# Optimization experiments

Measured on AMD Instinct MI355X. Metric: run time of the kernel, lower is better.

## Reference

```python
import jax, jax.numpy as jnp
import numpy as np

N_NODES, N_EDGES, N_GRAPHS = 50000, 500000, 64
NODE_D, EDGE_D, GLOB_D = 256, 128, 64
EPS = 1e-5


def setup_inputs() -> dict:
    key = jax.random.key(0)
    ks = jax.random.split(key, 12)
    inp = {
        "x": jax.random.normal(ks[0], (N_NODES, NODE_D), jnp.float32),
        "edge_attr": jax.random.normal(ks[1], (N_EDGES, EDGE_D), jnp.float32),
        "u": jax.random.normal(ks[2], (N_GRAPHS, GLOB_D), jnp.float32),
        "W1": jax.random.normal(ks[3], (NODE_D + EDGE_D, 4 * EDGE_D), jnp.float32) * 0.02,
        "b1": jnp.zeros((4 * EDGE_D,), jnp.float32),
        "W2": jax.random.normal(ks[4], (4 * EDGE_D, EDGE_D), jnp.float32) * 0.02,
        "b2": jnp.zeros((EDGE_D,), jnp.float32),
        "W3": jax.random.normal(ks[5], (NODE_D + EDGE_D + GLOB_D, 4 * NODE_D), jnp.float32) * 0.02,
        "b3": jnp.zeros((4 * NODE_D,), jnp.float32),
        "W4": jax.random.normal(ks[6], (4 * NODE_D, NODE_D), jnp.float32) * 0.02,
        "b4": jnp.zeros((NODE_D,), jnp.float32),
        "gamma": jnp.ones((NODE_D,), jnp.float32),
        "beta": jnp.zeros((NODE_D,), jnp.float32),
        "edge_index": jax.random.randint(ks[7], (2, N_EDGES), 0, N_NODES, jnp.int64 if jax.config.jax_enable_x64 else jnp.int32),
        "batch": jnp.sort(jax.random.randint(ks[8], (N_NODES,), 0, N_GRAPHS, jnp.int64 if jax.config.jax_enable_x64 else jnp.int32)),
    }
    return inp


def reference(x, edge_attr, u, W1, b1, W2, b2, W3, b3, W4, b4, gamma, beta, edge_index, batch):
    row, col = edge_index[0], edge_index[1]
    n = x.shape[0]
    # edge MLP on [x[row] || edge_attr]
    e = jnp.concatenate([x[row], edge_attr], axis=1)            # [E, node+edge]
    e = jnp.maximum(e @ W1 + b1, 0.0) @ W2 + b2                 # [E, edge]
    # scatter-mean by destination node
    s = jax.ops.segment_sum(e, col, num_segments=n)             # [N, edge]
    cnt = jax.ops.segment_sum(jnp.ones((col.shape[0],), x.dtype), col, num_segments=n)
    agg = s / jnp.maximum(cnt, 1.0)[:, None]
    # node update MLP on [x || agg || u[batch]]
    h = jnp.concatenate([x, agg, u[batch]], axis=1)             # [N, node+edge+glob]
    h = jnp.maximum(h @ W3 + b3, 0.0) @ W4 + b4                 # [N, node]
    # residual + layernorm (dropout p=0 -> identity)
    y = h + x
    mu = jnp.mean(y, axis=-1, keepdims=True)
    var = jnp.mean((y - mu) ** 2, axis=-1, keepdims=True)
    return (y - mu) * jax.lax.rsqrt(var + EPS) * gamma + beta
```

## Files before the change

### kernel.cpp

```cpp
#include <hip/hip_runtime.h>
#include <stdint.h>

#define NE 500000
#define NN 50000
#define ND 256
#define ED 128
#define GD 64
#define MAXDEG 64

typedef float f4v __attribute__((ext_vector_type(4)));
typedef short s8v __attribute__((ext_vector_type(8)));
typedef short s4v __attribute__((ext_vector_type(4)));

static __device__ __forceinline__ short f2bf(float f) {
  union { float f; uint32_t u; } v; v.f = f;
  uint32_t r = v.u + 0x7FFFu + ((v.u >> 16) & 1u);
  return (short)(r >> 16);
}
static __device__ __forceinline__ float bf2f(uint32_t u) {
  union { uint32_t u; float f; } v; v.u = u << 16; return v.f;
}

static __device__ __forceinline__ void pack_one(const float* __restrict__ src,
                                                short* __restrict__ dst, int C, int idx) {
  int k = idx / C, c = idx - k * C;
  int ks = k >> 5, kh = (k >> 3) & 3, j = k & 7;
  dst[(((ks * C + c) * 4 + kh) << 3) + j] = f2bf(src[idx]);
}

#define J0 3200000
#define J1 196608
#define J2 65536
#define J3 458752
#define J4 262144
#define J5 500000
__global__ void prep_kernel(const float* __restrict__ x, short* __restrict__ xbf,
                            const float* __restrict__ W1, const float* __restrict__ W2,
                            const float* __restrict__ W3, const float* __restrict__ W4,
                            short* __restrict__ w1p, short* __restrict__ w2p,
                            short* __restrict__ w3p, short* __restrict__ w4p,
                            const int* __restrict__ ecol, unsigned int* __restrict__ cnt,
                            int* __restrict__ elist) {
  int idx = blockIdx.x * blockDim.x + threadIdx.x;
  if (idx < J0) {
    int i = idx * 4;
    const float4 v = *(const float4*)(x + i);
    s4v o; o[0] = f2bf(v.x); o[1] = f2bf(v.y); o[2] = f2bf(v.z); o[3] = f2bf(v.w);
    *(s4v*)(xbf + i) = o;
    return;
  }
  idx -= J0;
  if (idx < J1) { pack_one(W1, w1p, 512, idx); return; }
  idx -= J1;
  if (idx < J2) { pack_one(W2, w2p, 128, idx); return; }
  idx -= J2;
  if (idx < J3) { pack_one(W3, w3p, 1024, idx); return; }
  idx -= J3;
  if (idx < J4) { pack_one(W4, w4p, 256, idx); return; }
  idx -= J4;
  if (idx < J5) {
    int c = ecol[idx];
    unsigned int slot = atomicAdd(&cnt[c], 1u);
    if (slot < MAXDEG) elist[c * MAXDEG + slot] = idx;
  }
}

__global__ void agg_kernel(const unsigned short* __restrict__ ebuf,
                           const int* __restrict__ elist,
                           const unsigned int* __restrict__ cnt,
                           unsigned short* __restrict__ aggbf) {
  int tid = threadIdx.x;
  int lane = tid & 63;
  int node = blockIdx.x * 4 + (tid >> 6);
  if (node >= NN) return;
  unsigned int deg = cnt[node];
  unsigned int jend = deg < MAXDEG ? deg : MAXDEG;
  float a0 = 0.f, a1 = 0.f;
  const int* el = elist + (size_t)node * MAXDEG;
  for (unsigned int j = 0; j < jend; ++j) {
    int eid = el[j];
    uint32_t v = *(const uint32_t*)(ebuf + (size_t)eid * ED + 2 * lane);
    a0 += bf2f(v & 0xFFFFu);
    a1 += bf2f(v >> 16);
  }
  float rc = 1.0f / (deg > 0 ? (float)deg : 1.0f);
  uint32_t o = (uint32_t)(uint16_t)f2bf(a0 * rc) | ((uint32_t)(uint16_t)f2bf(a1 * rc) << 16);
  *(uint32_t*)(aggbf + (size_t)node * ED + 2 * lane) = o;
}

__launch_bounds__(1024, 4)
__global__ void edge_kernel(const short* __restrict__ xbf,
                            const float* __restrict__ edge_attr,
                            const short* __restrict__ w1p,
                            const float* __restrict__ b1,
                            const short* __restrict__ w2p,
                            const float* __restrict__ b2,
                            const int* __restrict__ erow,
                            unsigned short* __restrict__ ebuf) {
  __shared__ __align__(16) short smem[128 * 384 + 128 * 256];
  char* const h1b = (char*)smem + 128 * 384 * 2;
  int* const rid = (int*)h1b;
  const int tid = threadIdx.x;
  const int lane = tid & 63;
  const int w = tid >> 6;
  const int lh = lane >> 4;
  const int ll = lane & 15;
  const int e0 = blockIdx.x * 128;

  if (tid < 128) {
    int e = e0 + tid;
    rid[tid] = (e < NE) ? erow[e] : 0;
  }
  __syncthreads();

  #pragma unroll
  for (int it = 0; it < 6; ++it) {
    int ch = tid + it * 1024;
    int rr = ch / 48;
    int cc = (ch - rr * 48) * 8;
    s8v vals = {0, 0, 0, 0, 0, 0, 0, 0};
    if (e0 + rr < NE) {
      if (cc < ND) {
        vals = *(const s8v*)(xbf + (size_t)rid[rr] * ND + cc);
      } else {
        const float* p = edge_attr + (size_t)(e0 + rr) * ED + (cc - ND);
        const float4 v0 = *(const float4*)(p);
        const float4 v1 = *(const float4*)(p + 4);
        vals[0] = f2bf(v0.x); vals[1] = f2bf(v0.y); vals[2] = f2bf(v0.z); vals[3] = f2bf(v0.w);
        vals[4] = f2bf(v1.x); vals[5] = f2bf(v1.y); vals[6] = f2bf(v1.z); vals[7] = f2bf(v1.w);
      }
    }
    int byte = (rr * 768 + cc * 2) ^ ((rr & 7) << 4);
    *(s8v*)((char*)smem + byte) = vals;
  }
  __syncthreads();

  f4v acc1[2][8];
  #pragma unroll
  for (int n = 0; n < 2; ++n)
    #pragma unroll
    for (int m = 0; m < 8; ++m)
      acc1[n][m] = (f4v){0.f, 0.f, 0.f, 0.f};

  for (int ks = 0; ks < 12; ++ks) {
    s8v wf0 = *(const s8v*)(w1p + (((ks * 512 + w * 16 + ll) * 4 + lh) << 3));
    s8v wf1 = *(const s8v*)(w1p + (((ks * 512 + 256 + w * 16 + ll) * 4 + lh) << 3));
    #pragma unroll
    for (int mh = 0; mh < 2; ++mh) {
      s8v hf[4];
      #pragma unroll
      for (int m = 0; m < 4; ++m) {
        int row = 64 * mh + 16 * m + ll;
        int byte = (row * 768 + ks * 64 + lh * 16) ^ ((row & 7) << 4);
        hf[m] = *(const s8v*)((const char*)smem + byte);
      }
      #pragma unroll
      for (int m = 0; m < 4; ++m) {
        acc1[0][4 * mh + m] = __builtin_amdgcn_mfma_f32_16x16x32_bf16(wf0, hf[m], acc1[0][4 * mh + m], 0, 0, 0);
        acc1[1][4 * mh + m] = __builtin_amdgcn_mfma_f32_16x16x32_bf16(wf1, hf[m], acc1[1][4 * mh + m], 0, 0, 0);
      }
    }
  }
  __syncthreads();

  f4v acc2[4];
  #pragma unroll
  for (int m = 0; m < 4; ++m)
    acc2[m] = (f4v){0.f, 0.f, 0.f, 0.f};

  #pragma unroll
  for (int half = 0; half < 2; ++half) {
    {
      int lcb = w * 16 + 4 * lh;
      const float4 bv = *(const float4*)(b1 + half * 256 + lcb);
      #pragma unroll
      for (int m = 0; m < 8; ++m) {
        int row = 16 * m + ll;
        s4v o;
        float v0 = acc1[half][m][0] + bv.x; o[0] = f2bf(v0 > 0.f ? v0 : 0.f);
        float v1 = acc1[half][m][1] + bv.y; o[1] = f2bf(v1 > 0.f ? v1 : 0.f);
        float v2 = acc1[half][m][2] + bv.z; o[2] = f2bf(v2 > 0.f ? v2 : 0.f);
        float v3 = acc1[half][m][3] + bv.w; o[3] = f2bf(v3 > 0.f ? v3 : 0.f);
        int byte = (row * 512 + lcb * 2) ^ ((row & 7) << 4);
        *(s4v*)(h1b + byte) = o;
      }
    }
    __syncthreads();

    for (int ksl = 0; ksl < 8; ++ksl) {
      int ksg = half * 8 + ksl;
      s8v wf = *(const s8v*)(w2p + (((ksg * 128 + (w & 7) * 16 + ll) * 4 + lh) << 3));
      #pragma unroll
      for (int m = 0; m < 4; ++m) {
        int row = 64 * (w >> 3) + 16 * m + ll;
        int byte = (row * 512 + ksl * 64 + lh * 16) ^ ((row & 7) << 4);
        s8v hf = *(const s8v*)(h1b + byte);
        acc2[m] = __builtin_amdgcn_mfma_f32_16x16x32_bf16(wf, hf, acc2[m], 0, 0, 0);
      }
    }
    __syncthreads();
  }

  {
    int cb = (w & 7) * 16 + 4 * lh;
    const float4 bv = *(const float4*)(b2 + cb);
    #pragma unroll
    for (int m = 0; m < 4; ++m) {
      int row = 64 * (w >> 3) + 16 * m + ll;
      s4v o;
      o[0] = f2bf(acc2[m][0] + bv.x);
      o[1] = f2bf(acc2[m][1] + bv.y);
      o[2] = f2bf(acc2[m][2] + bv.z);
      o[3] = f2bf(acc2[m][3] + bv.w);
      int byte = (row * 256 + cb * 2) ^ ((row & 7) << 4);
      *(s4v*)((char*)smem + byte) = o;
    }
  }
  __syncthreads();

  {
    size_t g0 = (size_t)e0 * ED;
    #pragma unroll
    for (int it = 0; it < 2; ++it) {
      int B = (tid + it * 1024) * 16;
      int row = B >> 8;
      int lb = B ^ ((row & 7) << 4);
      s8v v = *(const s8v*)((const char*)smem + lb);
      if (e0 + row < NE)
        *(s8v*)((char*)(ebuf + g0) + B) = v;
    }
  }
}

__launch_bounds__(1024, 4)
__global__ void node_kernel(const float* __restrict__ x,
                            const short* __restrict__ xbf,
                            const float* __restrict__ u,
                            const short* __restrict__ w3p,
                            const float* __restrict__ b3,
                            const short* __restrict__ w4p,
                            const float* __restrict__ b4,
                            const float* __restrict__ gamma,
                            const float* __restrict__ beta,
                            const int* __restrict__ batch,
                            const unsigned short* __restrict__ aggbf,
                            float* __restrict__ out) {
  __shared__ __align__(16) short smem[64 * 1024];
  const int tid = threadIdx.x;
  const int lane = tid & 63;
  const int w = tid >> 6;
  const int lh = lane >> 4;
  const int ll = lane & 15;
  const int n0 = blockIdx.x * 64;

  #pragma unroll
  for (int it = 0; it < 4; ++it) {
    int ch = tid + it * 1024;
    if (ch < 3584) {
      int rr = ch / 56;
      int cc = (ch - rr * 56) * 8;
      s8v vals = {0, 0, 0, 0, 0, 0, 0, 0};
      int node = n0 + rr;
      if (node < NN) {
        if (cc < 256) {
          vals = *(const s8v*)(xbf + (size_t)node * ND + cc);
        } else if (cc < 384) {
          vals = *(const s8v*)(aggbf + (size_t)node * ED + (cc - 256));
        } else {
          const float* up = u + (size_t)batch[node] * GD + (cc - 384);
          const float4 v0 = *(const float4*)(up);
          const float4 v1 = *(const float4*)(up + 4);
          vals[0] = f2bf(v0.x); vals[1] = f2bf(v0.y); vals[2] = f2bf(v0.z); vals[3] = f2bf(v0.w);
          vals[4] = f2bf(v1.x); vals[5] = f2bf(v1.y); vals[6] = f2bf(v1.z); vals[7] = f2bf(v1.w);
        }
      }
      int byte = (rr * 896 + cc * 2) ^ ((rr & 7) << 4);
      *(s8v*)((char*)smem + byte) = vals;
    }
  }
  __syncthreads();

  f4v acc3[4][4];
  #pragma unroll
  for (int n = 0; n < 4; ++n)
    #pragma unroll
    for (int m = 0; m < 4; ++m)
      acc3[n][m] = (f4v){0.f, 0.f, 0.f, 0.f};

  for (int ks = 0; ks < 14; ++ks) {
    s8v af[4];
    #pragma unroll
    for (int m = 0; m < 4; ++m) {
      int row = 16 * m + ll;
      int byte = (row * 896 + ks * 64 + lh * 16) ^ ((row & 7) << 4);
      af[m] = *(const s8v*)((const char*)smem + byte);
    }
    #pragma unroll
    for (int n = 0; n < 4; ++n) {
      s8v wf = *(const s8v*)(w3p + (((ks * 1024 + w * 64 + 16 * n + ll) * 4 + lh) << 3));
      #pragma unroll
      for (int m = 0; m < 4; ++m)
        acc3[n][m] = __builtin_amdgcn_mfma_f32_16x16x32_bf16(wf, af[m], acc3[n][m], 0, 0, 0);
    }
  }
  __syncthreads();

  #pragma unroll
  for (int n = 0; n < 4; ++n) {
    int cb = w * 64 + 16 * n + 4 * lh;
    const float4 bv = *(const float4*)(b3 + cb);
    #pragma unroll
    for (int m = 0; m < 4; ++m) {
      int row = 16 * m + ll;
      s4v o;
      float v0 = acc3[n][m][0] + bv.x; o[0] = f2bf(v0 > 0.f ? v0 : 0.f);
      float v1 = acc3[n][m][1] + bv.y; o[1] = f2bf(v1 > 0.f ? v1 : 0.f);
      float v2 = acc3[n][m][2] + bv.z; o[2] = f2bf(v2 > 0.f ? v2 : 0.f);
      float v3 = acc3[n][m][3] + bv.w; o[3] = f2bf(v3 > 0.f ? v3 : 0.f);
      int byte = (row * 2048 + cb * 2) ^ ((row & 7) << 4);
      *(s4v*)((char*)smem + byte) = o;
    }
  }
  __syncthreads();

  f4v acc4[4];
  #pragma unroll
  for (int m = 0; m < 4; ++m)
    acc4[m] = (f4v){0.f, 0.f, 0.f, 0.f};

  for (int ks = 0; ks < 32; ++ks) {
    s8v wf = *(const s8v*)(w4p + (((ks * 256 + w * 16 + ll) * 4 + lh) << 3));
    #pragma unroll
    for (int m = 0; m < 4; ++m) {
      int row = 16 * m + ll;
      int byte = (row * 2048 + ks * 64 + lh * 16) ^ ((row & 7) << 4);
      s8v hf = *(const s8v*)((const char*)smem + byte);
      acc4[m] = __builtin_amdgcn_mfma_f32_16x16x32_bf16(wf, hf, acc4[m], 0, 0, 0);
    }
  }
  __syncthreads();

  float* yb = (float*)smem;
  {
    int cb = w * 16 + 4 * lh;
    const float4 bv = *(const float4*)(b4 + cb);
    #pragma unroll
    for (int m = 0; m < 4; ++m) {
      int row = 16 * m + ll;
      int node = n0 + row;
      float4 xv = {0.f, 0.f, 0.f, 0.f};
      if (node < NN) xv = *(const float4*)(x + (size_t)node * ND + cb);
      f4v o;
      o[0] = acc4[m][0] + bv.x + xv.x;
      o[1] = acc4[m][1] + bv.y + xv.y;
      o[2] = acc4[m][2] + bv.z + xv.z;
      o[3] = acc4[m][3] + bv.w + xv.w;
      *(f4v*)(yb + row * 260 + cb) = o;
    }
  }
  __syncthreads();

  {
    int row = tid >> 4, sub = tid & 15;
    int node = n0 + row;
    float v[16];
    float sum = 0.f, ssq = 0.f;
    #pragma unroll
    for (int i = 0; i < 4; ++i) {
      const float4 t = *(const float4*)(yb + row * 260 + (i * 16 + sub) * 4);
      v[i * 4 + 0] = t.x; v[i * 4 + 1] = t.y; v[i * 4 + 2] = t.z; v[i * 4 + 3] = t.w;
      sum += t.x + t.y + t.z + t.w;
      ssq += t.x * t.x + t.y * t.y + t.z * t.z + t.w * t.w;
    }
    #pragma unroll
    for (int d = 1; d < 16; d <<= 1) {
      sum += __shfl_xor(sum, d);
      ssq += __shfl_xor(ssq, d);
    }
    float mu = sum * (1.f / 256.f);
    float var = ssq * (1.f / 256.f) - mu * mu;
    float rstd = rsqrtf(var + 1e-5f);
    if (node < NN) {
      #pragma unroll
      for (int i = 0; i < 4; ++i) {
        int c = (i * 16 + sub) * 4;
        const float4 g = *(const float4*)(gamma + c);
        const float4 be = *(const float4*)(beta + c);
        float4 o;
        o.x = (v[i * 4 + 0] - mu) * rstd * g.x + be.x;
        o.y = (v[i * 4 + 1] - mu) * rstd * g.y + be.y;
        o.z = (v[i * 4 + 2] - mu) * rstd * g.z + be.z;
        o.w = (v[i * 4 + 3] - mu) * rstd * g.w + be.w;
        *(float4*)(out + (size_t)node * ND + c) = o;
      }
    }
  }
}

extern "C" void kernel_launch(void* const* d_in, const int* in_sizes, int n_in,
                              void* d_out, int out_size, void* d_ws, size_t ws_size,
                              hipStream_t stream) {
  const float* x    = (const float*)d_in[0];
  const float* ea   = (const float*)d_in[1];
  const float* u    = (const float*)d_in[2];
  const float* W1   = (const float*)d_in[3];
  const float* b1   = (const float*)d_in[4];
  const float* W2   = (const float*)d_in[5];
  const float* b2   = (const float*)d_in[6];
  const float* W3   = (const float*)d_in[7];
  const float* b3   = (const float*)d_in[8];
  const float* W4   = (const float*)d_in[9];
  const float* b4   = (const float*)d_in[10];
  const float* gamma = (const float*)d_in[11];
  const float* beta  = (const float*)d_in[12];
  const int* eidx   = (const int*)d_in[13];
  const int* batch  = (const int*)d_in[14];
  float* out = (float*)d_out;

  char* p = (char*)d_ws;
  size_t off = 0;
  auto take = [&](size_t n) { char* r = p + off; off = (off + n + 255) & ~(size_t)255; return r; };
  short* xbf = (short*)take((size_t)NN * ND * 2);
  short* w1p = (short*)take((size_t)384 * 512 * 2);
  short* w2p = (short*)take((size_t)512 * 128 * 2);
  short* w3p = (short*)take((size_t)448 * 1024 * 2);
  short* w4p = (short*)take((size_t)1024 * 256 * 2);
  unsigned int* cnt = (unsigned int*)take((size_t)NN * 4);
  int* elist = (int*)take((size_t)NN * MAXDEG * 4);
  unsigned short* aggbf = (unsigned short*)take((size_t)NN * ED * 2);
  unsigned short* ebuf = (unsigned short*)take((size_t)NE * ED * 2);

  const int* erow = eidx;
  const int* ecol = eidx + NE;

  hipMemsetAsync(cnt, 0, (size_t)NN * 4, stream);
  {
    const int total = J0 + J1 + J2 + J3 + J4 + J5;
    prep_kernel<<<(total + 255) / 256, 256, 0, stream>>>(x, xbf, W1, W2, W3, W4,
                                                         w1p, w2p, w3p, w4p,
                                                         ecol, cnt, elist);
  }
  edge_kernel<<<(NE + 127) / 128, 1024, 0, stream>>>(xbf, ea, w1p, b1, w2p, b2, erow, ebuf);
  agg_kernel<<<(NN + 3) / 4, 256, 0, stream>>>(ebuf, elist, cnt, aggbf);
  node_kernel<<<(NN + 63) / 64, 1024, 0, stream>>>(x, xbf, u, w3p, b3, w4p, b4,
                                                   gamma, beta, batch, aggbf, out);
}
```

Before: 729.5 us.

## Gather edge-kernel x rows directly into LDS and split buffers to drop barriers

The gathered x[row] rows are now loaded with global_load_lds straight into a dedicated, XOR-swizzled LDS region, bypassing registers. Edge_attr is converted into a separate region and H1 gets its own buffer, so the barrier between GEMM1 and the H1 write is removed. The final output is written directly from registers as 8-byte stores instead of being staged through LDS, which removes one more barrier. LDS use grows from 160KB to 160KB (same total), but the erow bounds check on the gather is dropped and the output stores become narrower.

```diff
diff --git a/kernel.cpp b/kernel.cpp
--- a/kernel.cpp
+++ b/kernel.cpp
@@ -19,6 +19,13 @@
 }
 static __device__ __forceinline__ float bf2f(uint32_t u) {
   union { uint32_t u; float f; } v; v.u = u << 16; return v.f;
+}
+
+static __device__ __forceinline__ void gload_lds16(const void* g, void* l) {
+  __builtin_amdgcn_global_load_lds(
+      (const __attribute__((address_space(1))) unsigned int*)g,
+      (__attribute__((address_space(3))) unsigned int*)l,
+      16, 0, 0);
 }
 
 static __device__ __forceinline__ void pack_one(const float* __restrict__ src,
@@ -97,9 +104,10 @@
                             const float* __restrict__ b2,
                             const int* __restrict__ erow,
                             unsigned short* __restrict__ ebuf) {
-  __shared__ __align__(16) short smem[128 * 384 + 128 * 256];
-  char* const h1b = (char*)smem + 128 * 384 * 2;
-  int* const rid = (int*)h1b;
+  __shared__ __align__(16) short smem[81920];
+  char* const Xb = (char*)smem;
+  char* const Eb = (char*)smem + 65536;
+  char* const Hb = (char*)smem + 98304;
   const int tid = threadIdx.x;
   const int lane = tid & 63;
   const int w = tid >> 6;
@@ -107,31 +115,30 @@
   const int ll = lane & 15;
   const int e0 = blockIdx.x * 128;
 
-  if (tid < 128) {
-    int e = e0 + tid;
-    rid[tid] = (e < NE) ? erow[e] : 0;
-  }
-  __syncthreads();
-
-  #pragma unroll
-  for (int it = 0; it < 6; ++it) {
-    int ch = tid + it * 1024;
-    int rr = ch / 48;
-    int cc = (ch - rr * 48) * 8;
+  {
+    #pragma unroll
+    for (int i = 0; i < 4; ++i) {
+      int p = w * 4 + i;
+      int row = 2 * p + (lane >> 5);
+      int rid = erow[e0 + row];
+      int cg = (lane & 31) ^ (row & 7);
+      gload_lds16(xbf + (size_t)rid * 256 + cg * 8, Xb + p * 1024);
+    }
+  }
+
+  #pragma unroll
+  for (int it = 0; it < 2; ++it) {
+    int id = tid + it * 1024;
+    int row = id >> 4, oct = id & 15;
     s8v vals = {0, 0, 0, 0, 0, 0, 0, 0};
-    if (e0 + rr < NE) {
-      if (cc < ND) {
-        vals = *(const s8v*)(xbf + (size_t)rid[rr] * ND + cc);
-      } else {
-        const float* p = edge_attr + (size_t)(e0 + rr) * ED + (cc - ND);
-        const float4 v0 = *(const float4*)(p);
-        const float4 v1 = *(const float4*)(p + 4);
-        vals[0] = f2bf(v0.x); vals[1] = f2bf(v0.y); vals[2] = f2bf(v0.z); vals[3] = f2bf(v0.w);
-        vals[4] = f2bf(v1.x); vals[5] = f2bf(v1.y); vals[6] = f2bf(v1.z); vals[7] = f2bf(v1.w);
-      }
-    }
-    int byte = (rr * 768 + cc * 2) ^ ((rr & 7) << 4);
-    *(s8v*)((char*)smem + byte) = vals;
+    if (e0 + row < NE) {
+      const float* p = edge_attr + (size_t)(e0 + row) * ED + oct * 8;
+      const float4 v0 = *(const float4*)(p);
+      const float4 v1 = *(const float4*)(p + 4);
+      vals[0] = f2bf(v0.x); vals[1] = f2bf(v0.y); vals[2] = f2bf(v0.z); vals[3] = f2bf(v0.w);
+      vals[4] = f2bf(v1.x); vals[5] = f2bf(v1.y); vals[6] = f2bf(v1.z); vals[7] = f2bf(v1.w);
+    }
+    *(s8v*)(Eb + row * 256 + ((oct ^ (row & 7)) << 4)) = vals;
   }
   __syncthreads();
 
@@ -142,7 +149,7 @@
     for (int m = 0; m < 8; ++m)
       acc1[n][m] = (f4v){0.f, 0.f, 0.f, 0.f};
 
-  for (int ks = 0; ks < 12; ++ks) {
+  for (int ks = 0; ks < 8; ++ks) {
     s8v wf0 = *(const s8v*)(w1p + (((ks * 512 + w * 16 + ll) * 4 + lh) << 3));
     s8v wf1 = *(const s8v*)(w1p + (((ks * 512 + 256 + w * 16 + ll) * 4 + lh) << 3));
     #pragma unroll
@@ -151,8 +158,8 @@
       #pragma unroll
       for (int m = 0; m < 4; ++m) {
         int row = 64 * mh + 16 * m + ll;
-        int byte = (row * 768 + ks * 64 + lh * 16) ^ ((row & 7) << 4);
-        hf[m] = *(const s8v*)((const char*)smem + byte);
+        int byte = row * 512 + (((ks * 4 + lh) ^ (row & 7)) << 4);
+        hf[m] = *(const s8v*)(Xb + byte);
       }
       #pragma unroll
       for (int m = 0; m < 4; ++m) {
@@ -161,44 +168,87 @@
       }
     }
   }
-  __syncthreads();
+  for (int ks = 8; ks < 12; ++ks) {
+    s8v wf0 = *(const s8v*)(w1p + (((ks * 512 + w * 16 + ll) * 4 + lh) << 3));
+    s8v wf1 = *(const s8v*)(w1p + (((ks * 512 + 256 + w * 16 + ll) * 4 + lh) << 3));
+    #pragma unroll
+    for (int mh = 0; mh < 2; ++mh) {
+      s8v hf[4];
+      #pragma unroll
+      for (int m = 0; m < 4; ++m) {
+        int row = 64 * mh + 16 * m + ll;
+        int byte = row * 256 + ((((ks - 8) * 4 + lh) ^ (row & 7)) << 4);
+        hf[m] = *(const s8v*)(Eb + byte);
+      }
+      #pragma unroll
+      for (int m = 0; m < 4; ++m) {
+        acc1[0][4 * mh + m] = __builtin_amdgcn_mfma_f32_16x16x32_bf16(wf0, hf[m], acc1[0][4 * mh + m], 0, 0, 0);
+        acc1[1][4 * mh + m] = __builtin_amdgcn_mfma_f32_16x16x32_bf16(wf1, hf[m], acc1[1][4 * mh + m], 0, 0, 0);
+      }
+    }
+  }
 
   f4v acc2[4];
   #pragma unroll
   for (int m = 0; m < 4; ++m)
     acc2[m] = (f4v){0.f, 0.f, 0.f, 0.f};
 
-  #pragma unroll
-  for (int half = 0; half < 2; ++half) {
-    {
-      int lcb = w * 16 + 4 * lh;
-      const float4 bv = *(const float4*)(b1 + half * 256 + lcb);
-      #pragma unroll
-      for (int m = 0; m < 8; ++m) {
-        int row = 16 * m + ll;
-        s4v o;
-        float v0 = acc1[half][m][0] + bv.x; o[0] = f2bf(v0 > 0.f ? v0 : 0.f);
-        float v1 = acc1[half][m][1] + bv.y; o[1] = f2bf(v1 > 0.f ? v1 : 0.f);
-        float v2 = acc1[half][m][2] + bv.z; o[2] = f2bf(v2 > 0.f ? v2 : 0.f);
-        float v3 = acc1[half][m][3] + bv.w; o[3] = f2bf(v3 > 0.f ? v3 : 0.f);
-        int byte = (row * 512 + lcb * 2) ^ ((row & 7) << 4);
-        *(s4v*)(h1b + byte) = o;
-      }
-    }
-    __syncthreads();
-
-    for (int ksl = 0; ksl < 8; ++ksl) {
-      int ksg = half * 8 + ksl;
-      s8v wf = *(const s8v*)(w2p + (((ksg * 128 + (w & 7) * 16 + ll) * 4 + lh) << 3));
-      #pragma unroll
-      for (int m = 0; m < 4; ++m) {
-        int row = 64 * (w >> 3) + 16 * m + ll;
-        int byte = (row * 512 + ksl * 64 + lh * 16) ^ ((row & 7) << 4);
-        s8v hf = *(const s8v*)(h1b + byte);
-        acc2[m] = __builtin_amdgcn_mfma_f32_16x16x32_bf16(wf, hf, acc2[m], 0, 0, 0);
-      }
-    }
-    __syncthreads();
+  {
+    int lcb = w * 16 + 4 * lh;
+    const float4 bv = *(const float4*)(b1 + lcb);
+    #pragma unroll
+    for (int m = 0; m < 8; ++m) {
+      int row = 16 * m + ll;
+      s4v o;
+      float v0 = acc1[0][m][0] + bv.x; o[0] = f2bf(v0 > 0.f ? v0 : 0.f);
+      float v1 = acc1[0][m][1] + bv.y; o[1] = f2bf(v1 > 0.f ? v1 : 0.f);
+      float v2 = acc1[0][m][2] + bv.z; o[2] = f2bf(v2 > 0.f ? v2 : 0.f);
+      float v3 = acc1[0][m][3] + bv.w; o[3] = f2bf(v3 > 0.f ? v3 : 0.f);
+      int byte = (row * 512 + lcb * 2) ^ ((row & 7) << 4);
+      *(s4v*)(Hb + byte) = o;
+    }
+  }
+  __syncthreads();
+
+  for (int ksl = 0; ksl < 8; ++ksl) {
+    s8v wf = *(const s8v*)(w2p + (((ksl * 128 + (w & 7) * 16 + ll) * 4 + lh) << 3));
+    #pragma unroll
+    for (int m = 0; m < 4; ++m) {
+      int row = 64 * (w >> 3) + 16 * m + ll;
+      int byte = (row * 512 + ksl * 64 + lh * 16) ^ ((row & 7) << 4);
+      s8v hf = *(const s8v*)(Hb + byte);
+      acc2[m] = __builtin_amdgcn_mfma_f32_16x16x32_bf16(wf, hf, acc2[m], 0, 0, 0);
+    }
+  }
+  __syncthreads();
+
+  {
+    int lcb = w * 16 + 4 * lh;
+    const float4 bv = *(const float4*)(b1 + 256 + lcb);
+    #pragma unroll
+    for (int m = 0; m < 8; ++m) {
+      int row = 16 * m + ll;
+      s4v o;
+      float v0 = acc1[1][m][0] + bv.x; o[0] = f2bf(v0 > 0.f ? v0 : 0.f);
+      float v1 = acc1[1][m][1] + bv.y; o[1] = f2bf(v1 > 0.f ? v1 : 0.f);
+      float v2 = acc1[1][m][2] + bv.z; o[2] = f2bf(v2 > 0.f ? v2 : 0.f);
+      float v3 = acc1[1][m][3] + bv.w; o[3] = f2bf(v3 > 0.f ? v3 : 0.f);
+      int byte = (row * 512 + lcb * 2) ^ ((row & 7) << 4);
+      *(s4v*)(Hb + byte) = o;
+    }
+  }
+  __syncthreads();
+
+  for (int ksl = 0; ksl < 8; ++ksl) {
+    int ksg = 8 + ksl;
+    s8v wf = *(const s8v*)(w2p + (((ksg * 128 + (w & 7) * 16 + ll) * 4 + lh) << 3));
+    #pragma unroll
+    for (int m = 0; m < 4; ++m) {
+      int row = 64 * (w >> 3) + 16 * m + ll;
+      int byte = (row * 512 + ksl * 64 + lh * 16) ^ ((row & 7) << 4);
+      s8v hf = *(const s8v*)(Hb + byte);
+      acc2[m] = __builtin_amdgcn_mfma_f32_16x16x32_bf16(wf, hf, acc2[m], 0, 0, 0);
+    }
   }
 
   {
@@ -207,27 +257,15 @@
     #pragma unroll
     for (int m = 0; m < 4; ++m) {
       int row = 64 * (w >> 3) + 16 * m + ll;
-      s4v o;
-      o[0] = f2bf(acc2[m][0] + bv.x);
-      o[1] = f2bf(acc2[m][1] + bv.y);
-      o[2] = f2bf(acc2[m][2] + bv.z);
-      o[3] = f2bf(acc2[m][3] + bv.w);
-      int byte = (row * 256 + cb * 2) ^ ((row & 7) << 4);
-      *(s4v*)((char*)smem + byte) = o;
-    }
-  }
-  __syncthreads();
-
-  {
-    size_t g0 = (size_t)e0 * ED;
-    #pragma unroll
-    for (int it = 0; it < 2; ++it) {
-      int B = (tid + it * 1024) * 16;
-      int row = B >> 8;
-      int lb = B ^ ((row & 7) << 4);
-      s8v v = *(const s8v*)((const char*)smem + lb);
-      if (e0 + row < NE)
-        *(s8v*)((char*)(ebuf + g0) + B) = v;
+      int e = e0 + row;
+      if (e < NE) {
+        s4v o;
+        o[0] = f2bf(acc2[m][0] + bv.x);
+        o[1] = f2bf(acc2[m][1] + bv.y);
+        o[2] = f2bf(acc2[m][2] + bv.z);
+        o[3] = f2bf(acc2[m][3] + bv.w);
+        *(s4v*)(ebuf + (size_t)e * ED + cb) = o;
+      }
     }
   }
 }
```

Result: faster. 696.1 us (-4.6%).

## Load edge-MLP operands directly from global and double-buffer hidden slices

Applied to the files above, without the earlier changes.

The edge kernel no longer stages the gathered [x[row] || edge_attr] tile in LDS. Each wave now loads its MFMA B-fragments straight from global memory, reading the bf16 node features by row index and converting edge_attr on the fly. The hidden layer is written to LDS in four 128-column slices using a two-buffer scheme, so writing the next slice overlaps the second GEMM on the current one, and the output is stored directly to global without an LDS round trip. This shrinks LDS use and removes several barriers, which could raise occupancy. In exchange, each of the 16 waves redundantly re-reads the gathered inputs from global/L2, and the direct output stores are narrower and less coalesced.

```diff
diff --git a/kernel.cpp b/kernel.cpp
--- a/kernel.cpp
+++ b/kernel.cpp
@@ -97,9 +97,7 @@
                             const float* __restrict__ b2,
                             const int* __restrict__ erow,
                             unsigned short* __restrict__ ebuf) {
-  __shared__ __align__(16) short smem[128 * 384 + 128 * 256];
-  char* const h1b = (char*)smem + 128 * 384 * 2;
-  int* const rid = (int*)h1b;
+  __shared__ __align__(16) short hs[2][128 * 128];
   const int tid = threadIdx.x;
   const int lane = tid & 63;
   const int w = tid >> 6;
@@ -107,34 +105,6 @@
   const int ll = lane & 15;
   const int e0 = blockIdx.x * 128;
 
-  if (tid < 128) {
-    int e = e0 + tid;
-    rid[tid] = (e < NE) ? erow[e] : 0;
-  }
-  __syncthreads();
-
-  #pragma unroll
-  for (int it = 0; it < 6; ++it) {
-    int ch = tid + it * 1024;
-    int rr = ch / 48;
-    int cc = (ch - rr * 48) * 8;
-    s8v vals = {0, 0, 0, 0, 0, 0, 0, 0};
-    if (e0 + rr < NE) {
-      if (cc < ND) {
-        vals = *(const s8v*)(xbf + (size_t)rid[rr] * ND + cc);
-      } else {
-        const float* p = edge_attr + (size_t)(e0 + rr) * ED + (cc - ND);
-        const float4 v0 = *(const float4*)(p);
-        const float4 v1 = *(const float4*)(p + 4);
-        vals[0] = f2bf(v0.x); vals[1] = f2bf(v0.y); vals[2] = f2bf(v0.z); vals[3] = f2bf(v0.w);
-        vals[4] = f2bf(v1.x); vals[5] = f2bf(v1.y); vals[6] = f2bf(v1.z); vals[7] = f2bf(v1.w);
-      }
-    }
-    int byte = (rr * 768 + cc * 2) ^ ((rr & 7) << 4);
-    *(s8v*)((char*)smem + byte) = vals;
-  }
-  __syncthreads();
-
   f4v acc1[2][8];
   #pragma unroll
   for (int n = 0; n < 2; ++n)
@@ -142,59 +112,79 @@
     for (int m = 0; m < 8; ++m)
       acc1[n][m] = (f4v){0.f, 0.f, 0.f, 0.f};
 
-  for (int ks = 0; ks < 12; ++ks) {
+  {
+    int rid[8];
+    #pragma unroll
+    for (int m = 0; m < 8; ++m) {
+      int e = e0 + 16 * m + ll;
+      rid[m] = erow[e < NE ? e : NE - 1];
+    }
+    for (int ks = 0; ks < 8; ++ks) {
+      s8v wf0 = *(const s8v*)(w1p + (((ks * 512 + w * 16 + ll) * 4 + lh) << 3));
+      s8v wf1 = *(const s8v*)(w1p + (((ks * 512 + 256 + w * 16 + ll) * 4 + lh) << 3));
+      #pragma unroll
+      for (int m = 0; m < 8; ++m) {
+        s8v hf = *(const s8v*)(xbf + (size_t)rid[m] * 256 + (ks * 4 + lh) * 8);
+        acc1[0][m] = __builtin_amdgcn_mfma_f32_16x16x32_bf16(wf0, hf, acc1[0][m], 0, 0, 0);
+        acc1[1][m] = __builtin_amdgcn_mfma_f32_16x16x32_bf16(wf1, hf, acc1[1][m], 0, 0, 0);
+      }
+    }
+  }
+
+  for (int ks = 8; ks < 12; ++ks) {
     s8v wf0 = *(const s8v*)(w1p + (((ks * 512 + w * 16 + ll) * 4 + lh) << 3));
     s8v wf1 = *(const s8v*)(w1p + (((ks * 512 + 256 + w * 16 + ll) * 4 + lh) << 3));
     #pragma unroll
-    for (int mh = 0; mh < 2; ++mh) {
-      s8v hf[4];
-      #pragma unroll
-      for (int m = 0; m < 4; ++m) {
-        int row = 64 * mh + 16 * m + ll;
-        int byte = (row * 768 + ks * 64 + lh * 16) ^ ((row & 7) << 4);
-        hf[m] = *(const s8v*)((const char*)smem + byte);
-      }
-      #pragma unroll
-      for (int m = 0; m < 4; ++m) {
-        acc1[0][4 * mh + m] = __builtin_amdgcn_mfma_f32_16x16x32_bf16(wf0, hf[m], acc1[0][4 * mh + m], 0, 0, 0);
-        acc1[1][4 * mh + m] = __builtin_amdgcn_mfma_f32_16x16x32_bf16(wf1, hf[m], acc1[1][4 * mh + m], 0, 0, 0);
-      }
-    }
-  }
-  __syncthreads();
-
-  f4v acc2[4];
-  #pragma unroll
-  for (int m = 0; m < 4; ++m)
-    acc2[m] = (f4v){0.f, 0.f, 0.f, 0.f};
-
-  #pragma unroll
-  for (int half = 0; half < 2; ++half) {
-    {
-      int lcb = w * 16 + 4 * lh;
-      const float4 bv = *(const float4*)(b1 + half * 256 + lcb);
+    for (int m = 0; m < 8; ++m) {
+      int e = e0 + 16 * m + ll;
+      const float* pe = edge_attr + (size_t)(e < NE ? e : NE - 1) * ED + ((ks - 8) * 4 + lh) * 8;
+      const float4 v0 = *(const float4*)(pe);
+      const float4 v1 = *(const float4*)(pe + 4);
+      s8v hf;
+      hf[0] = f2bf(v0.x); hf[1] = f2bf(v0.y); hf[2] = f2bf(v0.z); hf[3] = f2bf(v0.w);
+      hf[4] = f2bf(v1.x); hf[5] = f2bf(v1.y); hf[6] = f2bf(v1.z); hf[7] = f2bf(v1.w);
+      acc1[0][m] = __builtin_amdgcn_mfma_f32_16x16x32_bf16(wf0, hf, acc1[0][m], 0, 0, 0);
+      acc1[1][m] = __builtin_amdgcn_mfma_f32_16x16x32_bf16(wf1, hf, acc1[1][m], 0, 0, 0);
+    }
+  }
+
+  auto write_slice = [&](int s) {
+    if ((w >> 3) == (s & 1)) {
+      const int n = s >> 1;
+      const int lcb = (w & 7) * 16 + 4 * lh;
+      const float4 bv = *(const float4*)(b1 + s * 128 + lcb);
       #pragma unroll
       for (int m = 0; m < 8; ++m) {
         int row = 16 * m + ll;
         s4v o;
-        float v0 = acc1[half][m][0] + bv.x; o[0] = f2bf(v0 > 0.f ? v0 : 0.f);
-        float v1 = acc1[half][m][1] + bv.y; o[1] = f2bf(v1 > 0.f ? v1 : 0.f);
-        float v2 = acc1[half][m][2] + bv.z; o[2] = f2bf(v2 > 0.f ? v2 : 0.f);
-        float v3 = acc1[half][m][3] + bv.w; o[3] = f2bf(v3 > 0.f ? v3 : 0.f);
-        int byte = (row * 512 + lcb * 2) ^ ((row & 7) << 4);
-        *(s4v*)(h1b + byte) = o;
-      }
-    }
-    __syncthreads();
-
-    for (int ksl = 0; ksl < 8; ++ksl) {
-      int ksg = half * 8 + ksl;
+        float v0 = acc1[n][m][0] + bv.x; o[0] = f2bf(v0 > 0.f ? v0 : 0.f);
+        float v1 = acc1[n][m][1] + bv.y; o[1] = f2bf(v1 > 0.f ? v1 : 0.f);
+        float v2 = acc1[n][m][2] + bv.z; o[2] = f2bf(v2 > 0.f ? v2 : 0.f);
+        float v3 = acc1[n][m][3] + bv.w; o[3] = f2bf(v3 > 0.f ? v3 : 0.f);
+        int byte = (row * 256 + lcb * 2) ^ ((row & 7) << 4);
+        *(s4v*)((char*)hs[s & 1] + byte) = o;
+      }
+    }
+  };
+
+  write_slice(0);
+  __syncthreads();
+
+  f4v acc2[4];
+  #pragma unroll
+  for (int m = 0; m < 4; ++m)
+    acc2[m] = (f4v){0.f, 0.f, 0.f, 0.f};
+
+  for (int s = 0; s < 4; ++s) {
+    if (s < 3) write_slice(s + 1);
+    for (int ksl = 0; ksl < 4; ++ksl) {
+      int ksg = s * 4 + ksl;
       s8v wf = *(const s8v*)(w2p + (((ksg * 128 + (w & 7) * 16 + ll) * 4 + lh) << 3));
       #pragma unroll
       for (int m = 0; m < 4; ++m) {
         int row = 64 * (w >> 3) + 16 * m + ll;
-        int byte = (row * 512 + ksl * 64 + lh * 16) ^ ((row & 7) << 4);
-        s8v hf = *(const s8v*)(h1b + byte);
+        int byte = (row * 256 + ksl * 64 + lh * 16) ^ ((row & 7) << 4);
+        s8v hf = *(const s8v*)((char*)hs[s & 1] + byte);
         acc2[m] = __builtin_amdgcn_mfma_f32_16x16x32_bf16(wf, hf, acc2[m], 0, 0, 0);
       }
     }
@@ -207,27 +197,15 @@
     #pragma unroll
     for (int m = 0; m < 4; ++m) {
       int row = 64 * (w >> 3) + 16 * m + ll;
-      s4v o;
-      o[0] = f2bf(acc2[m][0] + bv.x);
-      o[1] = f2bf(acc2[m][1] + bv.y);
-      o[2] = f2bf(acc2[m][2] + bv.z);
-      o[3] = f2bf(acc2[m][3] + bv.w);
-      int byte = (row * 256 + cb * 2) ^ ((row & 7) << 4);
-      *(s4v*)((char*)smem + byte) = o;
-    }
-  }
-  __syncthreads();
-
-  {
-    size_t g0 = (size_t)e0 * ED;
-    #pragma unroll
-    for (int it = 0; it < 2; ++it) {
-      int B = (tid + it * 1024) * 16;
-      int row = B >> 8;
-      int lb = B ^ ((row & 7) << 4);
-      s8v v = *(const s8v*)((const char*)smem + lb);
-      if (e0 + row < NE)
-        *(s8v*)((char*)(ebuf + g0) + B) = v;
+      int e = e0 + row;
+      if (e < NE) {
+        s4v o;
+        o[0] = f2bf(acc2[m][0] + bv.x);
+        o[1] = f2bf(acc2[m][1] + bv.y);
+        o[2] = f2bf(acc2[m][2] + bv.z);
+        o[3] = f2bf(acc2[m][3] + bv.w);
+        *(s4v*)(ebuf + (size_t)e * ED + cb) = o;
+      }
     }
   }
 }
```

Measured after the change: 1.500 ms. +105.6%, slower.
